# Kernel tuning notes

Hardware: AMD Instinct MI355X
Metric: run time of the kernel (lower is better)

The kernel has to match this reference:

```python
import jax, jax.numpy as jnp
import numpy as np

N_NODES = 50000
N_EDGES = 800000
IN_FEATS = 128
H_FEATS = 128


def setup_inputs() -> dict:
    key = jax.random.key(0)
    ks = jax.random.split(key, 5)
    x = jax.random.normal(ks[0], (N_NODES, IN_FEATS), dtype=jnp.float32)
    edge_index = jax.random.randint(ks[1], (2, N_EDGES), 0, N_NODES, dtype=jnp.int32)
    # Glorot-style init for the linear weights (as in PyG GCNConv)
    W1 = jax.random.normal(ks[2], (IN_FEATS, H_FEATS), dtype=jnp.float32) * (1.0 / np.sqrt(IN_FEATS))
    b1 = jnp.zeros((H_FEATS,), dtype=jnp.float32)
    W2 = jax.random.normal(ks[3], (H_FEATS, 1), dtype=jnp.float32) * (1.0 / np.sqrt(H_FEATS))
    b2 = jnp.zeros((1,), dtype=jnp.float32)
    return {"x": x, "edge_index": edge_index, "W1": W1, "b1": b1, "W2": W2, "b2": b2}


def reference(x, edge_index, W1, b1, W2, b2):
    N = x.shape[0]
    # --- GCN normalization (PyG GCNConv defaults): add self-loops, sym norm ---
    loop = jnp.arange(N, dtype=edge_index.dtype)
    src = jnp.concatenate([edge_index[0], loop])  # [E+N]
    dst = jnp.concatenate([edge_index[1], loop])  # [E+N]
    deg = jax.ops.segment_sum(jnp.ones_like(dst, dtype=x.dtype), dst, num_segments=N)
    deg_inv_sqrt = jax.lax.rsqrt(jnp.maximum(deg, 1.0))  # deg >= 1 w/ self-loops
    norm = deg_inv_sqrt[src] * deg_inv_sqrt[dst]          # [E+N]

    def gcn_conv(h, W, b):
        h = h @ W                                  # dense linear [N, out]
        msg = h[src] * norm[:, None]               # gather + scale [E+N, out]
        agg = jax.ops.segment_sum(msg, dst, num_segments=N)  # scatter-add
        return agg + b

    h = jax.nn.relu(gcn_conv(x, W1, b1))
    # dropout is identity in eval mode (training=False)
    out = gcn_conv(h, W2, b2).reshape(-1)  # [N]
    return out
```

## Files before the change

### kernel.cpp

```cpp
#include <hip/hip_runtime.h>
#include <hip/hip_bf16.h>

#define NN 50000
#define NE 800000
#define NF 128
#define NB 196
#define BSH 8
#define BNODES 256
#define GTILES 3125
#define HBLK 196
#define GBLK 784

typedef __attribute__((ext_vector_type(8))) short bf16x8;
typedef __attribute__((ext_vector_type(4))) float f32x4;
union Frag { uint4 u; bf16x8 v; };

__device__ __forceinline__ unsigned bf16rne(float f) {
    unsigned u = __float_as_uint(f);
    return (u + 0x7FFFu + ((u >> 16) & 1u)) >> 16;
}
__device__ __forceinline__ unsigned pk2(float lo, float hi) {
    __hip_bfloat162 h = __float22bfloat162_rn(float2{lo, hi});
    unsigned r; __builtin_memcpy(&r, &h, 4); return r;
}
__device__ __forceinline__ float blo(unsigned u) { return __uint_as_float(u << 16); }
__device__ __forceinline__ float bhi(unsigned u) { return __uint_as_float(u & 0xffff0000u); }

__global__ void zero_kernel(unsigned* __restrict__ hist) {
    if (threadIdx.x < NB) hist[threadIdx.x] = 0;
}

__global__ __launch_bounds__(256, 2) void histgemm_kernel(const int* __restrict__ ei,
                                                          unsigned* __restrict__ hist,
                                                          const float* __restrict__ x,
                                                          const float* __restrict__ W1,
                                                          unsigned short* __restrict__ H1u,
                                                          int E) {
    __shared__ unsigned lh[NB];
    __shared__ __align__(16) unsigned short w1t[128 * 128];
    const int t = threadIdx.x;

    if (blockIdx.x < HBLK) {
        if (t < NB) lh[t] = 0;
        __syncthreads();
        const int base = blockIdx.x * 4096;
#pragma unroll
        for (int j = 0; j < 16; ++j) {
            int e = base + j * 256 + t;
            if (e < E) atomicAdd(&lh[(unsigned)ei[E + e] >> BSH], 1u);
        }
        __syncthreads();
        if (t < NB && lh[t]) atomicAdd(&hist[t], lh[t]);
        return;
    }

    const int lane = t & 63;
    const int wid = t >> 6;

    {
        const int c = t & 127;
        const int kb0 = (t >> 7) * 8;
        char* wb = reinterpret_cast<char*>(w1t);
        for (int jj = 0; jj < 8; ++jj) {
            int k0 = kb0 + jj * 16;
            unsigned u0 = pk2(W1[(k0 + 0) * NF + c], W1[(k0 + 1) * NF + c]);
            unsigned u1 = pk2(W1[(k0 + 2) * NF + c], W1[(k0 + 3) * NF + c]);
            unsigned u2 = pk2(W1[(k0 + 4) * NF + c], W1[(k0 + 5) * NF + c]);
            unsigned u3 = pk2(W1[(k0 + 6) * NF + c], W1[(k0 + 7) * NF + c]);
            int off = (c * 256 + k0 * 2) ^ ((c & 7) << 4);
            *reinterpret_cast<uint4*>(wb + off) = make_uint4(u0, u1, u2, u3);
        }
    }
    __syncthreads();

    const int col = lane & 15;
    const int kb  = lane >> 4;
    const int cw  = wid * 32;
    Frag bfr[2][4];
    {
        const char* wb = reinterpret_cast<const char*>(w1t);
#pragma unroll
        for (int ct = 0; ct < 2; ++ct) {
            int c = cw + ct * 16 + col;
#pragma unroll
            for (int ks = 0; ks < 4; ++ks) {
                int k0 = ks * 32 + kb * 8;
                int off = (c * 256 + k0 * 2) ^ ((c & 7) << 4);
                bfr[ct][ks].u = *reinterpret_cast<const uint4*>(wb + off);
            }
        }
    }

    const int row = lane & 15;
    for (int tile = blockIdx.x - HBLK; tile < GTILES; tile += GBLK) {
        const int rb = tile * 16;
        const float* xr = x + (size_t)(rb + row) * NF + kb * 8;
        Frag a[4];
#pragma unroll
        for (int ks = 0; ks < 4; ++ks) {
            float4 q0 = *reinterpret_cast<const float4*>(xr + ks * 32);
            float4 q1 = *reinterpret_cast<const float4*>(xr + ks * 32 + 4);
            a[ks].u = make_uint4(pk2(q0.x, q0.y), pk2(q0.z, q0.w),
                                 pk2(q1.x, q1.y), pk2(q1.z, q1.w));
        }
        f32x4 acc0 = {0.f, 0.f, 0.f, 0.f};
        f32x4 acc1 = {0.f, 0.f, 0.f, 0.f};
#pragma unroll
        for (int ks = 0; ks < 4; ++ks) {
            acc0 = __builtin_amdgcn_mfma_f32_16x16x32_bf16(a[ks].v, bfr[0][ks].v, acc0, 0, 0, 0);
            acc1 = __builtin_amdgcn_mfma_f32_16x16x32_bf16(a[ks].v, bfr[1][ks].v, acc1, 0, 0, 0);
        }
        const int orow = rb + (lane >> 4) * 4;
#pragma unroll
        for (int r = 0; r < 4; ++r) {
            H1u[(size_t)(orow + r) * NF + cw + col]      = (unsigned short)bf16rne(acc0[r]);
            H1u[(size_t)(orow + r) * NF + cw + 16 + col] = (unsigned short)bf16rne(acc1[r]);
        }
    }
}

__global__ void bscan_kernel(const unsigned* __restrict__ hist, unsigned* __restrict__ boff,
                             unsigned* __restrict__ gcursor, int* __restrict__ row_ptr) {
    int lane = threadIdx.x & 63;
    unsigned v[4]; unsigned s = 0;
#pragma unroll
    for (int j = 0; j < 4; ++j) {
        int i = lane * 4 + j;
        v[j] = (i < NB) ? hist[i] : 0u;
        s += v[j];
    }
    unsigned e = s;
    for (int d = 1; d < 64; d <<= 1) {
        unsigned t = __shfl_up(e, d, 64);
        if (lane >= d) e += t;
    }
    e -= s;
    unsigned run = e;
#pragma unroll
    for (int j = 0; j < 4; ++j) {
        int i = lane * 4 + j;
        if (i < NB) { boff[i] = run; gcursor[i] = run; }
        run += v[j];
    }
    if (lane == 63) row_ptr[NN] = (int)run;
}

__global__ __launch_bounds__(256) void scatter_kernel(const int* __restrict__ ei,
                                                      unsigned* __restrict__ gcursor,
                                                      unsigned* __restrict__ bedge, int E) {
    __shared__ unsigned rec[8192];
    __shared__ unsigned char bkt[8192];
    __shared__ unsigned lh[NB], cb[NB], lh2[NB];
    const int t = threadIdx.x;
    if (t < NB) { lh[t] = 0; lh2[t] = 0; }
    __syncthreads();
    const int base = blockIdx.x * 8192;
    const int cnt = min(8192, E - base);
#pragma unroll
    for (int j = 0; j < 32; ++j) {
        int k = j * 256 + t;
        if (k < cnt) {
            int e = base + k;
            unsigned s = (unsigned)ei[e];
            unsigned d = (unsigned)ei[E + e];
            unsigned b = d >> BSH;
            rec[k] = (s << 8) | (d & 255u);
            bkt[k] = (unsigned char)b;
            atomicAdd(&lh[b], 1u);
        }
    }
    __syncthreads();
    if (t < NB) cb[t] = lh[t] ? atomicAdd(&gcursor[t], lh[t]) : 0u;
    __syncthreads();
#pragma unroll
    for (int j = 0; j < 32; ++j) {
        int k = j * 256 + t;
        if (k < cnt) {
            unsigned b = bkt[k];
            unsigned r = atomicAdd(&lh2[b], 1u);
            bedge[cb[b] + r] = rec[k];
        }
    }
}

__global__ __launch_bounds__(256) void csr_kernel(const unsigned* __restrict__ bedge,
                                                  const unsigned* __restrict__ boff,
                                                  const unsigned* __restrict__ bend,
                                                  int* __restrict__ row_ptr,
                                                  float* __restrict__ dis,
                                                  unsigned short* __restrict__ esrc) {
    __shared__ unsigned cnt[BNODES], woff[BNODES], cur[BNODES];
    __shared__ unsigned srec[8192];
    __shared__ unsigned short sout[8192];
    const int b = blockIdx.x;
    const unsigned base = boff[b];
    const unsigned end  = bend[b];
    const int ecnt = (int)(end - base);
    const int n0 = b * BNODES;
    const int nCnt = min(BNODES, NN - n0);
    const int t = threadIdx.x;
    cnt[t] = 0;
    __syncthreads();

    const bool fast = (ecnt <= 8192);
    if (fast) {
        for (int k = t; k < ecnt; k += 256) {
            unsigned r = bedge[base + k];
            srec[k] = r;
            atomicAdd(&cnt[r & 255u], 1u);
        }
    } else {
        for (int k = t; k < ecnt; k += 256) atomicAdd(&cnt[bedge[base + k] & 255u], 1u);
    }
    __syncthreads();
    if (t < 64) {
        unsigned v[4]; unsigned s = 0;
#pragma unroll
        for (int j = 0; j < 4; ++j) { v[j] = cnt[t * 4 + j]; s += v[j]; }
        unsigned e = s;
        for (int d = 1; d < 64; d <<= 1) {
            unsigned x = __shfl_up(e, d, 64);
            if (t >= d) e += x;
        }
        e -= s;
        unsigned run = e;
#pragma unroll
        for (int j = 0; j < 4; ++j) { woff[t * 4 + j] = run; run += v[j]; }
    }
    __syncthreads();
    if (t < nCnt) {
        row_ptr[n0 + t] = (int)(base + woff[t]);
        dis[n0 + t] = rsqrtf((float)(cnt[t] + 1u));
    }
    cur[t] = 0;
    __syncthreads();
    if (fast) {
        for (int k = t; k < ecnt; k += 256) {
            unsigned r = srec[k];
            unsigned dl = r & 255u;
            unsigned p = woff[dl] + atomicAdd(&cur[dl], 1u);
            sout[p] = (unsigned short)(r >> 8);
        }
        __syncthreads();
        for (int k = t; k < ecnt; k += 256) esrc[base + k] = sout[k];
    } else {
        for (int k = t; k < ecnt; k += 256) {
            unsigned r = bedge[base + k];
            unsigned dl = r & 255u;
            unsigned p = woff[dl] + atomicAdd(&cur[dl], 1u);
            esrc[base + p] = (unsigned short)(r >> 8);
        }
    }
}

__global__ __launch_bounds__(256) void layer1_kernel(const unsigned* __restrict__ H1b,
                                                     const unsigned short* __restrict__ esrc,
                                                     const int* __restrict__ row_ptr,
                                                     const float* __restrict__ dis,
                                                     const float* __restrict__ b1,
                                                     const float* __restrict__ W2,
                                                     float* __restrict__ zd, int N) {
    const int v = (blockIdx.x * 256 + threadIdx.x) >> 6;
    if (v >= N) return;
    const int lane = threadIdx.x & 63;
    const int quad = lane >> 4;
    const int s16  = lane & 15;
    const int base = row_ptr[v];
    const int end  = row_ptr[v + 1];
    const char* hb = reinterpret_cast<const char*>(H1b);

    float a[8];
#pragma unroll
    for (int k = 0; k < 8; ++k) a[k] = 0.f;

    for (int cb = base; cb < end; cb += 64) {
        const int m = min(64, end - cb);
        int es = 0; float ds_ = 0.f;
        if (cb + lane < end) {
            es = esrc[cb + lane];
            ds_ = dis[es];
        }
        const int nq = (m + 3) >> 2;
        int i = 0;
        for (; i + 4 <= nq; i += 4) {
            float w[4]; uint4 u[4];
#pragma unroll
            for (int j = 0; j < 4; ++j) {
                int idx = 4 * (i + j) + quad;
                int sj = __shfl(es, idx);
                w[j] = __shfl(ds_, idx);
                u[j] = *reinterpret_cast<const uint4*>(hb + (size_t)(unsigned)sj * 256 + s16 * 16);
            }
#pragma unroll
            for (int j = 0; j < 4; ++j) {
                a[0] = fmaf(blo(u[j].x), w[j], a[0]);
                a[1] = fmaf(bhi(u[j].x), w[j], a[1]);
                a[2] = fmaf(blo(u[j].y), w[j], a[2]);
                a[3] = fmaf(bhi(u[j].y), w[j], a[3]);
                a[4] = fmaf(blo(u[j].z), w[j], a[4]);
                a[5] = fmaf(bhi(u[j].z), w[j], a[5]);
                a[6] = fmaf(blo(u[j].w), w[j], a[6]);
                a[7] = fmaf(bhi(u[j].w), w[j], a[7]);
            }
        }
        for (; i < nq; ++i) {
            int idx = 4 * i + quad;
            int sj = __shfl(es, idx);
            float wj = __shfl(ds_, idx);
            uint4 uj = *reinterpret_cast<const uint4*>(hb + (size_t)(unsigned)sj * 256 + s16 * 16);
            a[0] = fmaf(blo(uj.x), wj, a[0]);
            a[1] = fmaf(bhi(uj.x), wj, a[1]);
            a[2] = fmaf(blo(uj.y), wj, a[2]);
            a[3] = fmaf(bhi(uj.y), wj, a[3]);
            a[4] = fmaf(blo(uj.z), wj, a[4]);
            a[5] = fmaf(bhi(uj.z), wj, a[5]);
            a[6] = fmaf(blo(uj.w), wj, a[6]);
            a[7] = fmaf(bhi(uj.w), wj, a[7]);
        }
    }

#pragma unroll
    for (int k = 0; k < 8; ++k) {
        a[k] += __shfl_xor(a[k], 16, 64);
        a[k] += __shfl_xor(a[k], 32, 64);
    }

    const float dv = dis[v];
    const float sw = dv * dv;
    uint4 hs = *reinterpret_cast<const uint4*>(hb + (size_t)v * 256 + s16 * 16);
    float hf[8] = { blo(hs.x), bhi(hs.x), blo(hs.y), bhi(hs.y),
                    blo(hs.z), bhi(hs.z), blo(hs.w), bhi(hs.w) };
    float4 bb0 = *reinterpret_cast<const float4*>(b1 + s16 * 8);
    float4 bb1 = *reinterpret_cast<const float4*>(b1 + s16 * 8 + 4);
    float4 w20 = *reinterpret_cast<const float4*>(W2 + s16 * 8);
    float4 w21 = *reinterpret_cast<const float4*>(W2 + s16 * 8 + 4);
    float bbv[8] = { bb0.x, bb0.y, bb0.z, bb0.w, bb1.x, bb1.y, bb1.z, bb1.w };
    float w2v[8] = { w20.x, w20.y, w20.z, w20.w, w21.x, w21.y, w21.z, w21.w };

    float p = 0.f;
#pragma unroll
    for (int k = 0; k < 8; ++k) {
        float h = fmaf(dv, a[k], fmaf(sw, hf[k], bbv[k]));
        h = h > 0.f ? h : 0.f;
        p = fmaf(h, w2v[k], p);
    }
    p += __shfl_xor(p, 1, 64);
    p += __shfl_xor(p, 2, 64);
    p += __shfl_xor(p, 4, 64);
    p += __shfl_xor(p, 8, 64);
    if (lane == 0) zd[v] = dv * p;
}

__global__ __launch_bounds__(256) void final_kernel(const float* __restrict__ zd,
                                                    const unsigned short* __restrict__ esrc,
                                                    const int* __restrict__ row_ptr,
                                                    const float* __restrict__ dis,
                                                    const float* __restrict__ b2,
                                                    float* __restrict__ out, int N) {
    const int g = (blockIdx.x * 256 + threadIdx.x) >> 3;
    if (g >= N) return;
    const int sl = threadIdx.x & 7;
    const int base = row_ptr[g];
    const int end  = row_ptr[g + 1];
    float acc = 0.f;
    for (int e = base + sl; e < end; e += 8) acc += zd[esrc[e]];
#pragma unroll
    for (int d = 1; d < 8; d <<= 1) acc += __shfl_xor(acc, d, 64);
    if (sl == 0) out[g] = fmaf(dis[g], acc + zd[g], b2[0]);
}

extern "C" void kernel_launch(void* const* d_in, const int* in_sizes, int n_in,
                              void* d_out, int out_size, void* d_ws, size_t ws_size,
                              hipStream_t stream) {
    const float* x  = (const float*)d_in[0];
    const int*   ei = (const int*)d_in[1];
    const float* W1 = (const float*)d_in[2];
    const float* b1 = (const float*)d_in[3];
    const float* W2 = (const float*)d_in[4];
    const float* b2 = (const float*)d_in[5];
    float* out = (float*)d_out;

    char* ws = (char*)d_ws;
    size_t o = 0;
    auto alloc = [&](size_t bytes) -> void* {
        void* p = ws + o;
        o += (bytes + 255) & ~(size_t)255;
        return p;
    };
    unsigned* hist    = (unsigned*)alloc((size_t)NB * 4);
    unsigned* boff    = (unsigned*)alloc((size_t)(NB + 1) * 4);
    unsigned* gcursor = (unsigned*)alloc((size_t)NB * 4);
    float*    dis     = (float*)alloc((size_t)NN * 4);
    int*      row_ptr = (int*)alloc((size_t)(NN + 1) * 4);
    unsigned* bedge   = (unsigned*)alloc((size_t)NE * 4);
    unsigned short* esrc = (unsigned short*)alloc((size_t)NE * 2);
    float*    zd      = (float*)alloc((size_t)NN * 4);
    unsigned* H1b     = (unsigned*)alloc((size_t)NN * NF * 2);

    zero_kernel<<<1, 256, 0, stream>>>(hist);
    histgemm_kernel<<<HBLK + GBLK, 256, 0, stream>>>(ei, hist, x, W1,
                                                     (unsigned short*)H1b, NE);
    bscan_kernel<<<1, 64, 0, stream>>>(hist, boff, gcursor, row_ptr);
    scatter_kernel<<<(NE + 8191) / 8192, 256, 0, stream>>>(ei, gcursor, bedge, NE);
    csr_kernel<<<NB, 256, 0, stream>>>(bedge, boff, gcursor, row_ptr, dis, esrc);

    layer1_kernel<<<(NN * 64 + 255) / 256, 256, 0, stream>>>(H1b, esrc, row_ptr, dis, b1, W2, zd, NN);

    final_kernel<<<(NN * 8 + 255) / 256, 256, 0, stream>>>(zd, esrc, row_ptr, dis, b2, out, NN);
}
```

Before: 92.92 us.

## Fuse histogram zeroing and bucket scan into histgemm via last-block reduction

Drops the zero and scan kernel launches. Each histogram block now writes its local counts to a per-block 2D array instead of atomically adding to a global histogram. The last block to finish, found through an atomicInc counter that wraps itself back to zero, reduces the columns and computes the exclusive scan. This removes two small kernel launches and their serialization gaps, at the cost of a threadfence and a serial reduction of 196x196 entries in one block. It relies on the done counter starting at zero in the workspace.

```diff
diff --git a/kernel.cpp b/kernel.cpp
--- a/kernel.cpp
+++ b/kernel.cpp
@@ -26,17 +26,18 @@
 __device__ __forceinline__ float blo(unsigned u) { return __uint_as_float(u << 16); }
 __device__ __forceinline__ float bhi(unsigned u) { return __uint_as_float(u & 0xffff0000u); }
 
-__global__ void zero_kernel(unsigned* __restrict__ hist) {
-    if (threadIdx.x < NB) hist[threadIdx.x] = 0;
-}
-
 __global__ __launch_bounds__(256, 2) void histgemm_kernel(const int* __restrict__ ei,
-                                                          unsigned* __restrict__ hist,
+                                                          unsigned* __restrict__ hist2d,
+                                                          unsigned* __restrict__ done,
                                                           const float* __restrict__ x,
                                                           const float* __restrict__ W1,
                                                           unsigned short* __restrict__ H1u,
+                                                          unsigned* __restrict__ boff,
+                                                          unsigned* __restrict__ gcursor,
+                                                          int* __restrict__ row_ptr,
                                                           int E) {
     __shared__ unsigned lh[NB];
+    __shared__ int winner;
     __shared__ __align__(16) unsigned short w1t[128 * 128];
     const int t = threadIdx.x;
 
@@ -50,7 +51,50 @@
             if (e < E) atomicAdd(&lh[(unsigned)ei[E + e] >> BSH], 1u);
         }
         __syncthreads();
-        if (t < NB && lh[t]) atomicAdd(&hist[t], lh[t]);
+        if (t < NB) hist2d[(size_t)t * HBLK + blockIdx.x] = lh[t];
+        __threadfence();
+        __syncthreads();
+        if (t == 0) {
+            unsigned old = atomicInc(done, 195u);
+            winner = (old == 194u);
+        }
+        __syncthreads();
+        if (winner) {
+            __threadfence();
+            if (t < 64) {
+                const int lane = t;
+                unsigned v[4]; unsigned s = 0;
+#pragma unroll
+                for (int j = 0; j < 4; ++j) {
+                    int b = lane * 4 + j;
+                    unsigned sum = 0;
+                    if (b < NB) {
+                        const uint4* p = reinterpret_cast<const uint4*>(hist2d + (size_t)b * HBLK);
+#pragma unroll 7
+                        for (int q = 0; q < HBLK / 4; ++q) {
+                            uint4 u = p[q];
+                            sum += u.x + u.y + u.z + u.w;
+                        }
+                    }
+                    v[j] = sum;
+                    s += sum;
+                }
+                unsigned e = s;
+                for (int d = 1; d < 64; d <<= 1) {
+                    unsigned tt = __shfl_up(e, d, 64);
+                    if (lane >= d) e += tt;
+                }
+                e -= s;
+                unsigned run = e;
+#pragma unroll
+                for (int j = 0; j < 4; ++j) {
+                    int b = lane * 4 + j;
+                    if (b < NB) { boff[b] = run; gcursor[b] = run; }
+                    run += v[j];
+                }
+                if (lane == 63) row_ptr[NN] = (int)run;
+            }
+        }
         return;
     }
 
@@ -117,32 +161,6 @@
             H1u[(size_t)(orow + r) * NF + cw + 16 + col] = (unsigned short)bf16rne(acc1[r]);
         }
     }
-}
-
-__global__ void bscan_kernel(const unsigned* __restrict__ hist, unsigned* __restrict__ boff,
-                             unsigned* __restrict__ gcursor, int* __restrict__ row_ptr) {
-    int lane = threadIdx.x & 63;
-    unsigned v[4]; unsigned s = 0;
-#pragma unroll
-    for (int j = 0; j < 4; ++j) {
-        int i = lane * 4 + j;
-        v[j] = (i < NB) ? hist[i] : 0u;
-        s += v[j];
-    }
-    unsigned e = s;
-    for (int d = 1; d < 64; d <<= 1) {
-        unsigned t = __shfl_up(e, d, 64);
-        if (lane >= d) e += t;
-    }
-    e -= s;
-    unsigned run = e;
-#pragma unroll
-    for (int j = 0; j < 4; ++j) {
-        int i = lane * 4 + j;
-        if (i < NB) { boff[i] = run; gcursor[i] = run; }
-        run += v[j];
-    }
-    if (lane == 63) row_ptr[NN] = (int)run;
 }
 
 __global__ __launch_bounds__(256) void scatter_kernel(const int* __restrict__ ei,
@@ -387,7 +405,8 @@
         o += (bytes + 255) & ~(size_t)255;
         return p;
     };
-    unsigned* hist    = (unsigned*)alloc((size_t)NB * 4);
+    unsigned* hist2d  = (unsigned*)alloc((size_t)NB * HBLK * 4);
+    unsigned* done    = (unsigned*)alloc(256);
     unsigned* boff    = (unsigned*)alloc((size_t)(NB + 1) * 4);
     unsigned* gcursor = (unsigned*)alloc((size_t)NB * 4);
     float*    dis     = (float*)alloc((size_t)NN * 4);
@@ -397,10 +416,9 @@
     float*    zd      = (float*)alloc((size_t)NN * 4);
     unsigned* H1b     = (unsigned*)alloc((size_t)NN * NF * 2);
 
-    zero_kernel<<<1, 256, 0, stream>>>(hist);
-    histgemm_kernel<<<HBLK + GBLK, 256, 0, stream>>>(ei, hist, x, W1,
-                                                     (unsigned short*)H1b, NE);
-    bscan_kernel<<<1, 64, 0, stream>>>(hist, boff, gcursor, row_ptr);
+    histgemm_kernel<<<HBLK + GBLK, 256, 0, stream>>>(ei, hist2d, done, x, W1,
+                                                     (unsigned short*)H1b,
+                                                     boff, gcursor, row_ptr, NE);
     scatter_kernel<<<(NE + 8191) / 8192, 256, 0, stream>>>(ei, gcursor, bedge, NE);
     csr_kernel<<<NB, 256, 0, stream>>>(bedge, boff, gcursor, row_ptr, dis, esrc);
 
```

Result: slower. 124.3 us (+33.7%).
